# Kernel optimization log

Measured on AMD Instinct MI355X. Metric: run time of the kernel, lower is better.

The kernel has to match this reference:

```python
import jax, jax.numpy as jnp
import numpy as np

E = 512      # embed_size
H = 8        # heads
HD = E // H  # head_dim
TN = 288     # time_num
FE = 4       # forward_expansion
N, T = 64, 512


def layernorm(x, g, b, eps=1e-5):
    mu = jnp.mean(x, axis=-1, keepdims=True)
    var = jnp.mean((x - mu) ** 2, axis=-1, keepdims=True)
    return (x - mu) * jax.lax.rsqrt(var + eps) * g + b


def setup_inputs() -> dict:
    key = jax.random.key(0)
    ks = jax.random.split(key, 12)
    w = lambda k, sh: jax.random.normal(k, sh, dtype=jnp.float32) * 0.02
    return {
        "value": jax.random.normal(ks[0], (N, T, E), dtype=jnp.float32),
        "key_in": jax.random.normal(ks[1], (N, T, E), dtype=jnp.float32),
        "query": jax.random.normal(ks[2], (N, T, E), dtype=jnp.float32),
        "i": 37,
        # One_hot_encoder params: learned identity-init table + linear to embed
        "I_mat": jnp.eye(TN, dtype=jnp.float32),
        "oh_W": w(ks[3], (TN, E)), "oh_b": jnp.zeros((E,), jnp.float32),
        # per-head projections (shared across heads, as in the torch module)
        "Wv": w(ks[4], (HD, HD)), "Wk": w(ks[5], (HD, HD)), "Wq": w(ks[6], (HD, HD)),
        "Wo": w(ks[7], (E, E)), "bo": jnp.zeros((E,), jnp.float32),
        "g1": jnp.ones((E,), jnp.float32), "b1": jnp.zeros((E,), jnp.float32),
        "g2": jnp.ones((E,), jnp.float32), "b2": jnp.zeros((E,), jnp.float32),
        "W1": w(ks[8], (E, FE * E)), "bf1": jnp.zeros((FE * E,), jnp.float32),
        "W2": w(ks[9], (FE * E, E)), "bf2": jnp.zeros((E,), jnp.float32),
    }


def reference(value, key_in, query, i, I_mat, oh_W, oh_b, Wv, Wk, Wq, Wo, bo,
              g1, b1, g2, b2, W1, bf1, W2, bf2):
    n, t, c = query.shape
    # One_hot_encoder: rows i..i+T-1 (mod time_num) of learned table -> linear
    rows = (i + jnp.arange(t)) % TN
    onehot = I_mat[rows] @ oh_W + oh_b            # (T, E), broadcast over N
    q_in = query + onehot[None, :, :]
    # per-head projections
    v = value.reshape(n, t, H, HD) @ Wv           # (N,T,H,HD)
    k = key_in.reshape(n, t, H, HD) @ Wk
    qh = q_in.reshape(n, t, H, HD) @ Wq
    # attention (note: scale uses sqrt(embed_size), per original code)
    energy = jnp.einsum("nqhd,nkhd->nhqk", qh, k) / jnp.sqrt(jnp.float32(E))
    attn = jax.nn.softmax(energy, axis=-1)
    out = jnp.einsum("nhqk,nkhd->nqhd", attn, v).reshape(n, t, E)
    out = out @ Wo + bo
    # residual + LN + FFN + residual + LN (dropout=0 -> identity)
    x = layernorm(out + q_in, g1, b1)
    ff = jax.nn.relu(x @ W1 + bf1) @ W2 + bf2
    return layernorm(ff + x, g2, b2)
```

## Files before the change

kernel.cpp:

```cpp
#include <hip/hip_runtime.h>

typedef __attribute__((ext_vector_type(8))) short s16x8;
typedef __attribute__((ext_vector_type(4))) float f32x4;

#define TN 288

__device__ __forceinline__ unsigned short f2bf(float f) {
  union { float f; unsigned u; } v; v.f = f;
  unsigned r = v.u + 0x7fffu + ((v.u >> 16) & 1u);
  return (unsigned short)(r >> 16);
}
__device__ __forceinline__ float bf2f(unsigned short u) {
  union { float f; unsigned u; } v; v.u = ((unsigned)u) << 16;
  return v.f;
}
__device__ __forceinline__ unsigned lds_addr(const void* p) {
  return (unsigned)(unsigned long long)(const __attribute__((address_space(3))) char*)p;
}
__device__ __forceinline__ void async_copy16(unsigned short* lds, const unsigned short* g) {
  __builtin_amdgcn_global_load_lds(
      (const __attribute__((address_space(1))) unsigned int*)g,
      (__attribute__((address_space(3))) unsigned int*)lds, 16, 0, 0);
}

__device__ __forceinline__ void pack_body(const float* __restrict__ W,
    unsigned short* __restrict__ out, int N, long t) {
  int lr = (int)(t & 15);
  int lg = (int)((t >> 4) & 3);
  long g6 = t >> 6;
  int nt = N >> 4;
  int n16 = (int)(g6 % nt);
  int kb = (int)(g6 / nt) << 5;
  int k = kb + lg * 8;
  int col = n16 * 16 + lr;
  s16x8 v;
#pragma unroll
  for (int j = 0; j < 8; ++j) v[j] = (short)f2bf(W[(size_t)(k + j) * N + col]);
  *(s16x8*)(out + t * 8) = v;
}

__global__ __launch_bounds__(256) void prep_kernel(const int* __restrict__ pi,
    const float* __restrict__ I_mat, const float* __restrict__ ohW,
    const float* __restrict__ ohb, float* __restrict__ onehot,
    const float* __restrict__ Wv, const float* __restrict__ Wk,
    const float* __restrict__ Wq, unsigned short* __restrict__ Wv_b,
    unsigned short* __restrict__ Wk_b, unsigned short* __restrict__ Wq_b,
    const float* __restrict__ Wo, const float* __restrict__ W1,
    const float* __restrict__ W2, unsigned short* __restrict__ Wop,
    unsigned short* __restrict__ W1p, unsigned short* __restrict__ W2p) {
  int b = blockIdx.x, tid = threadIdx.x;
  if (b < 512) {
    int t = b;
    int r = (pi[0] + t) % TN;
    float acc0 = ohb[tid], acc1 = ohb[tid + 256];
    const float* Ir = I_mat + (size_t)r * TN;
    for (int j = 0; j < TN; ++j) {
      float iv = Ir[j];
      acc0 += iv * ohW[(size_t)j * 512 + tid];
      acc1 += iv * ohW[(size_t)j * 512 + tid + 256];
    }
    onehot[(size_t)t * 512 + tid] = acc0;
    onehot[(size_t)t * 512 + tid + 256] = acc1;
  } else if (b < 640) {
    pack_body(Wo, Wop, 512, (long)(b - 512) * 256 + tid);
  } else if (b < 1152) {
    pack_body(W1, W1p, 2048, (long)(b - 640) * 256 + tid);
  } else if (b < 1664) {
    pack_body(W2, W2p, 512, (long)(b - 1152) * 256 + tid);
  } else {
    int which = b - 1664;
    const float* src = which == 0 ? Wv : (which == 1 ? Wk : Wq);
    unsigned short* dst = which == 0 ? Wv_b : (which == 1 ? Wk_b : Wq_b);
    float sc = which == 2 ? 0.06375871424f : 1.f;
#pragma unroll
    for (int j = 0; j < 4; ++j) {
      int i = tid * 16 + j * 4;
      float4 f = *(const float4*)(src + i);
      unsigned lo = (unsigned)f2bf(f.x * sc) | ((unsigned)f2bf(f.y * sc) << 16);
      unsigned hi = (unsigned)f2bf(f.z * sc) | ((unsigned)f2bf(f.w * sc) << 16);
      *(uint2*)(dst + i) = make_uint2(lo, hi);
    }
  }
}

template<bool QIN, int OUTMODE>
__global__ __launch_bounds__(256) void proj_gemm(const float* __restrict__ A,
    const unsigned short* __restrict__ B, const float* __restrict__ onehot,
    unsigned short* __restrict__ C, int M, int N, int K) {
  __shared__ unsigned short As[64][40];
  __shared__ unsigned short Bs[64][40];
  __shared__ unsigned short Cs[64][72];
  const int m0 = blockIdx.x * 64, n0 = blockIdx.y * 64;
  const int tid = threadIdx.x, w = tid >> 6, l = tid & 63, lr = l & 15, lg = l >> 4;
  const int wr = (w >> 1) * 32, wc = (w & 1) * 32;
  const int aRow = (tid * 8) >> 5, aK = (tid * 8) & 31;
  const int bK = (tid * 8) >> 6, bCol = (tid * 8) & 63;
  f32x4 acc[2][2] = {};
  for (int kb = 0; kb < K; kb += 32) {
    size_t fl = (size_t)(m0 + aRow) * K + kb + aK;
    float4 f0 = *(const float4*)(A + fl);
    float4 f1 = *(const float4*)(A + fl + 4);
    if (QIN) {
      const float* oh = onehot + (fl & 262143);
      float4 o0 = *(const float4*)(oh);
      float4 o1 = *(const float4*)(oh + 4);
      f0.x += o0.x; f0.y += o0.y; f0.z += o0.z; f0.w += o0.w;
      f1.x += o1.x; f1.y += o1.y; f1.z += o1.z; f1.w += o1.w;
    }
    s16x8 av;
    av[0] = (short)f2bf(f0.x); av[1] = (short)f2bf(f0.y);
    av[2] = (short)f2bf(f0.z); av[3] = (short)f2bf(f0.w);
    av[4] = (short)f2bf(f1.x); av[5] = (short)f2bf(f1.y);
    av[6] = (short)f2bf(f1.z); av[7] = (short)f2bf(f1.w);
    *(s16x8*)&As[aRow][aK] = av;
    s16x8 bv = *(const s16x8*)(B + (size_t)(kb + bK) * N + n0 + bCol);
#pragma unroll
    for (int j = 0; j < 8; ++j) Bs[bCol + j][bK] = (unsigned short)bv[j];
    __syncthreads();
    s16x8 af0 = *(const s16x8*)&As[wr + lr][lg * 8];
    s16x8 af1 = *(const s16x8*)&As[wr + 16 + lr][lg * 8];
    s16x8 bf0 = *(const s16x8*)&Bs[wc + lr][lg * 8];
    s16x8 bf1 = *(const s16x8*)&Bs[wc + 16 + lr][lg * 8];
    acc[0][0] = __builtin_amdgcn_mfma_f32_16x16x32_bf16(af0, bf0, acc[0][0], 0, 0, 0);
    acc[0][1] = __builtin_amdgcn_mfma_f32_16x16x32_bf16(af0, bf1, acc[0][1], 0, 0, 0);
    acc[1][0] = __builtin_amdgcn_mfma_f32_16x16x32_bf16(af1, bf0, acc[1][0], 0, 0, 0);
    acc[1][1] = __builtin_amdgcn_mfma_f32_16x16x32_bf16(af1, bf1, acc[1][1], 0, 0, 0);
    __syncthreads();
  }
  if (OUTMODE == 0) {
#pragma unroll
    for (int fi = 0; fi < 2; ++fi)
#pragma unroll
      for (int fj = 0; fj < 2; ++fj)
#pragma unroll
        for (int r = 0; r < 4; ++r) {
          int row = m0 + wr + fi * 16 + lg * 4 + r;
          int col = n0 + wc + fj * 16 + lr;
          C[(size_t)row * N + col] = f2bf(acc[fi][fj][r]);
        }
  } else {
#pragma unroll
    for (int fi = 0; fi < 2; ++fi)
#pragma unroll
      for (int fj = 0; fj < 2; ++fj)
#pragma unroll
        for (int r = 0; r < 4; ++r)
          Cs[wr + fi * 16 + lg * 4 + r][wc + fj * 16 + lr] = f2bf(acc[fi][fj][r]);
    __syncthreads();
    int nIdx = m0 >> 12, t0 = (m0 >> 3) & 511;
#pragma unroll
    for (int it = 0; it < 2; ++it) {
      int p = tid + it * 256;
      int hh = p >> 6, d = p & 63;
      s16x8 vv;
#pragma unroll
      for (int j = 0; j < 8; ++j) vv[j] = (short)Cs[j * 8 + hh][d];
      *(s16x8*)(C + (((size_t)(nIdx * 8 + hh) * 64 + d) << 9) + t0) = vv;
    }
  }
}

template<bool RELU, bool OUTBF>
__global__ __launch_bounds__(256) void gemmF(
    const unsigned short* __restrict__ A, int lda,
    const unsigned short* __restrict__ Bp, int ldbp, int nOff,
    const float* __restrict__ bias, void* __restrict__ Cout, int ldc,
    int M, int K, int nby) {
  __shared__ unsigned short As[2][8192];
  const int tid = threadIdx.x, w = tid >> 6, l = tid & 63, lr = l & 15, lg = l >> 4;
  const int nwg = gridDim.x;
  const int bid = (blockIdx.x & 7) * (nwg >> 3) + (blockIdx.x >> 3);
  const int bx = bid / nby, by = bid % nby;
  const int m0 = bx * 128;
  const int wr = (w >> 1) * 64, wc = (w & 1) * 64;
  const int srow = tid >> 3, sc8 = tid & 7;
  const int gcol = (sc8 ^ (srow & 7)) * 8;
  const unsigned short* Ag = A + (size_t)(m0 + srow) * lda + gcol;
  const size_t ldaa = (size_t)32 * lda;
  const unsigned short* Bg = Bp +
      ((size_t)(nOff >> 4) + by * 8 + (wc >> 4)) * 512 + lg * 128 + lr * 8;
  const size_t bks = (size_t)ldbp * 512;

  f32x4 acc[4][4] = {};
  s16x8 b0[4], b1[4];

#pragma unroll
  for (int it = 0; it < 4; ++it)
    async_copy16(&As[0][(it * 256 + tid) * 8], Ag + it * ldaa);
#pragma unroll
  for (int fj = 0; fj < 4; ++fj) {
    b0[fj] = *(const s16x8*)(Bg + fj * 512);
    b1[fj] = *(const s16x8*)(Bg + bks + fj * 512);
  }
  __syncthreads();

  int buf = 0;
  for (int kb = 0; kb < K; kb += 64) {
    int kn = (kb + 64 < K) ? kb + 64 : 0;
#pragma unroll
    for (int it = 0; it < 4; ++it)
      async_copy16(&As[buf ^ 1][(it * 256 + tid) * 8], Ag + kn + it * ldaa);
    s16x8 b0n[4];
    {
      const unsigned short* p = Bg + ((size_t)(kn >> 5)) * bks;
#pragma unroll
      for (int fj = 0; fj < 4; ++fj) b0n[fj] = *(const s16x8*)(p + fj * 512);
    }
    {
      s16x8 af[4];
#pragma unroll
      for (int fi = 0; fi < 4; ++fi) {
        int row = wr + fi * 16 + lr;
        af[fi] = *(const s16x8*)&As[buf][row * 64 + ((lg ^ (row & 7)) * 8)];
      }
#pragma unroll
      for (int fi = 0; fi < 4; ++fi)
#pragma unroll
        for (int fj = 0; fj < 4; ++fj)
          acc[fi][fj] = __builtin_amdgcn_mfma_f32_16x16x32_bf16(af[fi], b0[fj], acc[fi][fj], 0, 0, 0);
    }
    s16x8 b1n[4];
    {
      const unsigned short* p = Bg + ((size_t)((kn + 32) >> 5)) * bks;
#pragma unroll
      for (int fj = 0; fj < 4; ++fj) b1n[fj] = *(const s16x8*)(p + fj * 512);
    }
    {
      s16x8 af[4];
#pragma unroll
      for (int fi = 0; fi < 4; ++fi) {
        int row = wr + fi * 16 + lr;
        af[fi] = *(const s16x8*)&As[buf][row * 64 + (((4 + lg) ^ (row & 7)) * 8)];
      }
#pragma unroll
      for (int fi = 0; fi < 4; ++fi)
#pragma unroll
        for (int fj = 0; fj < 4; ++fj)
          acc[fi][fj] = __builtin_amdgcn_mfma_f32_16x16x32_bf16(af[fi], b1[fj], acc[fi][fj], 0, 0, 0);
    }
    __syncthreads();
#pragma unroll
    for (int fj = 0; fj < 4; ++fj) { b0[fj] = b0n[fj]; b1[fj] = b1n[fj]; }
    buf ^= 1;
  }

#pragma unroll
  for (int fj = 0; fj < 4; ++fj) {
    int colL = by * 128 + wc + fj * 16 + lr;
    float bv = bias[nOff + colL];
#pragma unroll
    for (int fi = 0; fi < 4; ++fi)
#pragma unroll
      for (int r = 0; r < 4; ++r) {
        int row = m0 + wr + fi * 16 + lg * 4 + r;
        size_t ci = (size_t)row * ldc + colL;
        float v = acc[fi][fj][r] + bv;
        if (RELU) v = fmaxf(v, 0.f);
        if (OUTBF) ((unsigned short*)Cout)[ci] = f2bf(v);
        else ((float*)Cout)[ci] = v;
      }
  }
}

__global__ __launch_bounds__(256, 2) void attn_kernel(
    const unsigned short* __restrict__ Qp, const unsigned short* __restrict__ Kp,
    const unsigned short* __restrict__ Vt, unsigned short* __restrict__ Out) {
  __shared__ unsigned short KS[128][72];
  __shared__ unsigned short P[4][16][132];
  const int bid = blockIdx.x;
  const int qh = bid >> 9, g = bid & 511, h = g & 7, n = g >> 3;
  const int tid = threadIdx.x, w = tid >> 6, l = tid & 63, lr = l & 15, lg = l >> 4;
  const int q0 = qh * 256;

  s16x8 qf[4][2];
#pragma unroll
  for (int rt = 0; rt < 4; ++rt) {
    const size_t qb = (((size_t)(n * 512 + q0 + w * 64 + rt * 16 + lr)) * 8 + h) * 64;
    qf[rt][0] = *(const s16x8*)(Qp + qb + lg * 8);
    qf[rt][1] = *(const s16x8*)(Qp + qb + 32 + lg * 8);
  }
  const unsigned short* Vb = Vt + ((size_t)(n * 8 + h)) * 32768 + (size_t)lr * 512 + lg * 8;

  f32x4 oacc[4][4] = {};
  float m[4][4], lsum[4][4];
#pragma unroll
  for (int rt = 0; rt < 4; ++rt)
#pragma unroll
    for (int r = 0; r < 4; ++r) { m[rt][r] = -1e30f; lsum[rt][r] = 0.f; }
  s16x8 vreg[16];

#pragma unroll
  for (int it = 0; it < 4; ++it) {
    int idx = tid + it * 256;
    int rr = idx >> 3, dd = (idx & 7) * 8;
    *(s16x8*)&KS[rr][dd] =
        *(const s16x8*)(Kp + (((size_t)(n * 512 + rr)) * 8 + h) * 64 + dd);
  }
#pragma unroll
  for (int ks = 0; ks < 4; ++ks)
#pragma unroll
    for (int fj = 0; fj < 4; ++fj)
      vreg[ks * 4 + fj] = *(const s16x8*)(Vb + fj * 8192 + ks * 32);
  __syncthreads();

  for (int c = 0; c < 4; ++c) {
    if (c) {
      __syncthreads();
#pragma unroll
      for (int it = 0; it < 4; ++it) {
        int idx = tid + it * 256;
        int rr = idx >> 3, dd = (idx & 7) * 8;
        *(s16x8*)&KS[rr][dd] =
            *(const s16x8*)(Kp + (((size_t)(n * 512 + c * 128 + rr)) * 8 + h) * 64 + dd);
      }
#pragma unroll
      for (int ks = 0; ks < 4; ++ks)
#pragma unroll
        for (int fj = 0; fj < 4; ++fj)
          vreg[ks * 4 + fj] = *(const s16x8*)(Vb + fj * 8192 + c * 128 + ks * 32);
      __syncthreads();
    }
#pragma unroll
    for (int rt = 0; rt < 4; ++rt) {
      f32x4 sacc[8];
      __builtin_amdgcn_s_setprio(1);
#pragma unroll
      for (int f = 0; f < 8; ++f) {
        s16x8 b0 = *(const s16x8*)&KS[f * 16 + lr][lg * 8];
        s16x8 b1 = *(const s16x8*)&KS[f * 16 + lr][32 + lg * 8];
        f32x4 a = {};
        a = __builtin_amdgcn_mfma_f32_16x16x32_bf16(qf[rt][0], b0, a, 0, 0, 0);
        a = __builtin_amdgcn_mfma_f32_16x16x32_bf16(qf[rt][1], b1, a, 0, 0, 0);
        sacc[f] = a;
      }
      __builtin_amdgcn_s_setprio(0);

      float fs[4];
#pragma unroll
      for (int r = 0; r < 4; ++r) {
        float cm = sacc[0][r];
#pragma unroll
        for (int f = 1; f < 8; ++f) cm = fmaxf(cm, sacc[f][r]);
#pragma unroll
        for (int mk = 1; mk < 16; mk <<= 1) cm = fmaxf(cm, __shfl_xor(cm, mk));
        float mn = fmaxf(m[rt][r], cm);
        fs[r] = __builtin_amdgcn_exp2f(m[rt][r] - mn);
        m[rt][r] = mn;
        unsigned pa = lds_addr(&P[w][lg * 4 + r][lr]);
        float cs = 0.f;
#pragma unroll
        for (int f = 0; f < 8; ++f) {
          float p = __builtin_amdgcn_exp2f(sacc[f][r] - mn);
          asm volatile("ds_write_b16_d16_hi %0, %1 offset:%2"
                       :: "v"(pa), "v"(p), "i"(f * 32) : "memory");
          cs += p;
        }
#pragma unroll
        for (int mk = 1; mk < 16; mk <<= 1) cs += __shfl_xor(cs, mk);
        lsum[rt][r] = lsum[rt][r] * fs[r] + cs;
      }
#pragma unroll
      for (int fj = 0; fj < 4; ++fj)
#pragma unroll
        for (int r = 0; r < 4; ++r) oacc[rt][fj][r] *= fs[r];

      asm volatile("s_waitcnt lgkmcnt(0)" ::: "memory");
      __builtin_amdgcn_sched_barrier(0);
      __builtin_amdgcn_s_setprio(1);
#pragma unroll
      for (int ks = 0; ks < 4; ++ks) {
        s16x8 pa = *(const s16x8*)&P[w][lr][ks * 32 + lg * 8];
#pragma unroll
        for (int fj = 0; fj < 4; ++fj)
          oacc[rt][fj] = __builtin_amdgcn_mfma_f32_16x16x32_bf16(pa, vreg[ks * 4 + fj], oacc[rt][fj], 0, 0, 0);
      }
      __builtin_amdgcn_s_setprio(0);
    }
  }

#pragma unroll
  for (int rt = 0; rt < 4; ++rt)
#pragma unroll
    for (int fj = 0; fj < 4; ++fj)
#pragma unroll
      for (int r = 0; r < 4; ++r) {
        int qrow = q0 + w * 64 + rt * 16 + lg * 4 + r;
        Out[((size_t)(n * 512 + qrow)) * 512 + h * 64 + fj * 16 + lr] =
            f2bf(oacc[rt][fj][r] / lsum[rt][r]);
      }
}

template<bool XBF, bool RBF, bool QIN, bool OUTBF>
__global__ __launch_bounds__(256) void ln_kernel(const void* __restrict__ Xv,
    const void* __restrict__ Rv, const float* __restrict__ onehot,
    const float* __restrict__ g, const float* __restrict__ bb,
    void* __restrict__ outv) {
  int row = blockIdx.x * 4 + (threadIdx.x >> 6);
  int l = threadIdx.x & 63;
  size_t base = (size_t)row * 512 + l * 8;
  float v[8];
  if (XBF) {
    s16x8 xv = *(const s16x8*)((const unsigned short*)Xv + base);
#pragma unroll
    for (int j = 0; j < 8; ++j) v[j] = bf2f((unsigned short)xv[j]);
  } else {
    const float* X = (const float*)Xv;
    float4 x0 = *(const float4*)(X + base);
    float4 x1 = *(const float4*)(X + base + 4);
    v[0] = x0.x; v[1] = x0.y; v[2] = x0.z; v[3] = x0.w;
    v[4] = x1.x; v[5] = x1.y; v[6] = x1.z; v[7] = x1.w;
  }
  if (RBF) {
    s16x8 rv = *(const s16x8*)((const unsigned short*)Rv + base);
#pragma unroll
    for (int j = 0; j < 8; ++j) v[j] += bf2f((unsigned short)rv[j]);
  } else {
    const float* R = (const float*)Rv;
    float4 r0 = *(const float4*)(R + base);
    float4 r1 = *(const float4*)(R + base + 4);
    v[0] += r0.x; v[1] += r0.y; v[2] += r0.z; v[3] += r0.w;
    v[4] += r1.x; v[5] += r1.y; v[6] += r1.z; v[7] += r1.w;
  }
  if (QIN) {
    size_t ob = (size_t)(row & 511) * 512 + l * 8;
    float4 o0 = *(const float4*)(onehot + ob);
    float4 o1 = *(const float4*)(onehot + ob + 4);
    v[0] += o0.x; v[1] += o0.y; v[2] += o0.z; v[3] += o0.w;
    v[4] += o1.x; v[5] += o1.y; v[6] += o1.z; v[7] += o1.w;
  }
  float s = 0.f, ss = 0.f;
#pragma unroll
  for (int j = 0; j < 8; ++j) { s += v[j]; ss += v[j] * v[j]; }
#pragma unroll
  for (int mk = 1; mk < 64; mk <<= 1) { s += __shfl_xor(s, mk); ss += __shfl_xor(ss, mk); }
  float mu = s * (1.f / 512.f);
  float inv = rsqrtf(ss * (1.f / 512.f) - mu * mu + 1e-5f);
#pragma unroll
  for (int j = 0; j < 8; ++j) {
    int e = l * 8 + j;
    float y = (v[j] - mu) * inv * g[e] + bb[e];
    if (OUTBF) ((unsigned short*)outv)[base + j] = f2bf(y);
    else ((float*)outv)[base + j] = y;
  }
}

extern "C" void kernel_launch(void* const* d_in, const int* in_sizes, int n_in,
                              void* d_out, int out_size, void* d_ws, size_t ws_size,
                              hipStream_t stream) {
  const float* value  = (const float*)d_in[0];
  const float* key_in = (const float*)d_in[1];
  const float* query  = (const float*)d_in[2];
  const int*   pi     = (const int*)d_in[3];
  const float* I_mat  = (const float*)d_in[4];
  const float* ohW    = (const float*)d_in[5];
  const float* ohb    = (const float*)d_in[6];
  const float* Wv     = (const float*)d_in[7];
  const float* Wk     = (const float*)d_in[8];
  const float* Wq     = (const float*)d_in[9];
  const float* Wo     = (const float*)d_in[10];
  const float* bo     = (const float*)d_in[11];
  const float* g1     = (const float*)d_in[12];
  const float* b1     = (const float*)d_in[13];
  const float* g2     = (const float*)d_in[14];
  const float* b2     = (const float*)d_in[15];
  const float* W1     = (const float*)d_in[16];
  const float* bf1    = (const float*)d_in[17];
  const float* W2     = (const float*)d_in[18];
  const float* bf2    = (const float*)d_in[19];

  char* ws = (char*)d_ws;
  const size_t MB = 1024 * 1024;
  unsigned short* q_p  = (unsigned short*)d_out;
  unsigned short* k_p  = q_p + 16777216;
  unsigned short* vT     = (unsigned short*)(ws + 0);
  unsigned short* attn_o = (unsigned short*)(ws + 32 * MB);
  unsigned short* x_b    = (unsigned short*)(ws + 64 * MB);
  unsigned short* ff1h   = (unsigned short*)(ws + 0);
  float*          onehot = (float*)(ws + 96 * MB);
  unsigned short* Wv_b   = (unsigned short*)(ws + 97 * MB);
  unsigned short* Wk_b   = Wv_b + 4096;
  unsigned short* Wq_b   = Wk_b + 4096;
  unsigned short* Wop    = Wq_b + 4096;
  unsigned short* W1p    = Wop + 262144;
  unsigned short* W2p    = W1p + 1048576;

  prep_kernel<<<1667, 256, 0, stream>>>(pi, I_mat, ohW, ohb, onehot,
      Wv, Wk, Wq, Wv_b, Wk_b, Wq_b, Wo, W1, W2, Wop, W1p, W2p);

  dim3 gp(4096, 1);
  proj_gemm<false, 1><<<gp, 256, 0, stream>>>(value,  Wv_b, nullptr, vT,  262144, 64, 64);
  proj_gemm<false, 0><<<gp, 256, 0, stream>>>(key_in, Wk_b, nullptr, k_p, 262144, 64, 64);
  proj_gemm<true,  0><<<gp, 256, 0, stream>>>(query,  Wq_b, onehot,  q_p, 262144, 64, 64);

  attn_kernel<<<1024, 256, 0, stream>>>(q_p, k_p, vT, attn_o);

  gemmF<false, true><<<1024, 256, 0, stream>>>(
      attn_o, 512, Wop, 32, 0, bo, x_b, 512, 32768, 512, 4);
  ln_kernel<true, false, true, true><<<8192, 256, 0, stream>>>(x_b, query, onehot, g1, b1, x_b);

  for (int hf = 0; hf < 2; ++hf) {
    const unsigned short* xh = x_b + (size_t)hf * 16384 * 512;
    gemmF<true, true><<<2048, 256, 0, stream>>>(
        xh, 512, W1p, 128, 0, bf1, ff1h, 2048, 16384, 512, 16);
    gemmF<false, false><<<512, 256, 0, stream>>>(
        ff1h, 2048, W2p, 32, 0, bf2, (float*)d_out + (size_t)hf * 16384 * 512, 512, 16384, 2048, 4);
  }
  ln_kernel<false, true, false, false><<<8192, 256, 0, stream>>>(d_out, x_b, nullptr, g2, b2, d_out);
}
```

Baseline: 468.3 us.

## Merge projection launches, fuse FFN residual into GEMM epilogue, skip unit rescale

Replaces the three projection GEMM launches with one kernel that picks value, key or query from the block index. The second FFN GEMM now adds the bf16 residual in its epilogue, so the final layernorm no longer reads the residual tensor. The attention kernel skips rescaling the output accumulators when every correction factor in the wavefront is exactly one. The aim is fewer launches, less residual traffic and fewer multiplies, at the cost of runtime branching in the projection kernel and a wave-vote check in the softmax loop.

```diff
diff --git a/kernel.cpp b/kernel.cpp
--- a/kernel.cpp
+++ b/kernel.cpp
@@ -83,24 +83,32 @@
   }
 }
 
-template<bool QIN, int OUTMODE>
-__global__ __launch_bounds__(256) void proj_gemm(const float* __restrict__ A,
-    const unsigned short* __restrict__ B, const float* __restrict__ onehot,
-    unsigned short* __restrict__ C, int M, int N, int K) {
+__global__ __launch_bounds__(256) void proj_all(
+    const float* __restrict__ value, const float* __restrict__ key_in,
+    const float* __restrict__ query, const unsigned short* __restrict__ Wv_b,
+    const unsigned short* __restrict__ Wk_b, const unsigned short* __restrict__ Wq_b,
+    const float* __restrict__ onehot, unsigned short* __restrict__ vT,
+    unsigned short* __restrict__ k_p, unsigned short* __restrict__ q_p) {
   __shared__ unsigned short As[64][40];
   __shared__ unsigned short Bs[64][40];
   __shared__ unsigned short Cs[64][72];
-  const int m0 = blockIdx.x * 64, n0 = blockIdx.y * 64;
+  const int which = blockIdx.x >> 12;
+  const int mb = blockIdx.x & 4095;
+  const float* A = which == 0 ? value : (which == 1 ? key_in : query);
+  const unsigned short* B = which == 0 ? Wv_b : (which == 1 ? Wk_b : Wq_b);
+  unsigned short* C = which == 0 ? vT : (which == 1 ? k_p : q_p);
+  const bool qin = (which == 2);
+  const int m0 = mb * 64;
   const int tid = threadIdx.x, w = tid >> 6, l = tid & 63, lr = l & 15, lg = l >> 4;
   const int wr = (w >> 1) * 32, wc = (w & 1) * 32;
   const int aRow = (tid * 8) >> 5, aK = (tid * 8) & 31;
   const int bK = (tid * 8) >> 6, bCol = (tid * 8) & 63;
   f32x4 acc[2][2] = {};
-  for (int kb = 0; kb < K; kb += 32) {
-    size_t fl = (size_t)(m0 + aRow) * K + kb + aK;
+  for (int kb = 0; kb < 64; kb += 32) {
+    size_t fl = (size_t)(m0 + aRow) * 64 + kb + aK;
     float4 f0 = *(const float4*)(A + fl);
     float4 f1 = *(const float4*)(A + fl + 4);
-    if (QIN) {
+    if (qin) {
       const float* oh = onehot + (fl & 262143);
       float4 o0 = *(const float4*)(oh);
       float4 o1 = *(const float4*)(oh + 4);
@@ -113,7 +121,7 @@
     av[4] = (short)f2bf(f1.x); av[5] = (short)f2bf(f1.y);
     av[6] = (short)f2bf(f1.z); av[7] = (short)f2bf(f1.w);
     *(s16x8*)&As[aRow][aK] = av;
-    s16x8 bv = *(const s16x8*)(B + (size_t)(kb + bK) * N + n0 + bCol);
+    s16x8 bv = *(const s16x8*)(B + (size_t)(kb + bK) * 64 + bCol);
 #pragma unroll
     for (int j = 0; j < 8; ++j) Bs[bCol + j][bK] = (unsigned short)bv[j];
     __syncthreads();
@@ -127,7 +135,7 @@
     acc[1][1] = __builtin_amdgcn_mfma_f32_16x16x32_bf16(af1, bf1, acc[1][1], 0, 0, 0);
     __syncthreads();
   }
-  if (OUTMODE == 0) {
+  if (which != 0) {
 #pragma unroll
     for (int fi = 0; fi < 2; ++fi)
 #pragma unroll
@@ -135,8 +143,8 @@
 #pragma unroll
         for (int r = 0; r < 4; ++r) {
           int row = m0 + wr + fi * 16 + lg * 4 + r;
-          int col = n0 + wc + fj * 16 + lr;
-          C[(size_t)row * N + col] = f2bf(acc[fi][fj][r]);
+          int col = wc + fj * 16 + lr;
+          C[(size_t)row * 64 + col] = f2bf(acc[fi][fj][r]);
         }
   } else {
 #pragma unroll
@@ -160,11 +168,12 @@
   }
 }
 
-template<bool RELU, bool OUTBF>
+template<bool RELU, bool OUTBF, bool RES>
 __global__ __launch_bounds__(256) void gemmF(
     const unsigned short* __restrict__ A, int lda,
     const unsigned short* __restrict__ Bp, int ldbp, int nOff,
-    const float* __restrict__ bias, void* __restrict__ Cout, int ldc,
+    const float* __restrict__ bias, void* __restrict__ Cout,
+    const unsigned short* __restrict__ resid, int ldc,
     int M, int K, int nby) {
   __shared__ unsigned short As[2][8192];
   const int tid = threadIdx.x, w = tid >> 6, l = tid & 63, lr = l & 15, lg = l >> 4;
@@ -255,6 +264,7 @@
         int row = m0 + wr + fi * 16 + lg * 4 + r;
         size_t ci = (size_t)row * ldc + colL;
         float v = acc[fi][fj][r] + bv;
+        if (RES) v += bf2f(resid[ci]);
         if (RELU) v = fmaxf(v, 0.f);
         if (OUTBF) ((unsigned short*)Cout)[ci] = f2bf(v);
         else ((float*)Cout)[ci] = v;
@@ -359,10 +369,12 @@
         for (int mk = 1; mk < 16; mk <<= 1) cs += __shfl_xor(cs, mk);
         lsum[rt][r] = lsum[rt][r] * fs[r] + cs;
       }
-#pragma unroll
-      for (int fj = 0; fj < 4; ++fj)
-#pragma unroll
-        for (int r = 0; r < 4; ++r) oacc[rt][fj][r] *= fs[r];
+      if (!__all(fs[0] == 1.f && fs[1] == 1.f && fs[2] == 1.f && fs[3] == 1.f)) {
+#pragma unroll
+        for (int fj = 0; fj < 4; ++fj)
+#pragma unroll
+          for (int r = 0; r < 4; ++r) oacc[rt][fj][r] *= fs[r];
+      }
 
       asm volatile("s_waitcnt lgkmcnt(0)" ::: "memory");
       __builtin_amdgcn_sched_barrier(0);
@@ -390,7 +402,7 @@
       }
 }
 
-template<bool XBF, bool RBF, bool QIN, bool OUTBF>
+template<bool XBF, bool RES, bool RBF, bool QIN, bool OUTBF>
 __global__ __launch_bounds__(256) void ln_kernel(const void* __restrict__ Xv,
     const void* __restrict__ Rv, const float* __restrict__ onehot,
     const float* __restrict__ g, const float* __restrict__ bb,
@@ -410,16 +422,18 @@
     v[0] = x0.x; v[1] = x0.y; v[2] = x0.z; v[3] = x0.w;
     v[4] = x1.x; v[5] = x1.y; v[6] = x1.z; v[7] = x1.w;
   }
-  if (RBF) {
-    s16x8 rv = *(const s16x8*)((const unsigned short*)Rv + base);
-#pragma unroll
-    for (int j = 0; j < 8; ++j) v[j] += bf2f((unsigned short)rv[j]);
-  } else {
-    const float* R = (const float*)Rv;
-    float4 r0 = *(const float4*)(R + base);
-    float4 r1 = *(const float4*)(R + base + 4);
-    v[0] += r0.x; v[1] += r0.y; v[2] += r0.z; v[3] += r0.w;
-    v[4] += r1.x; v[5] += r1.y; v[6] += r1.z; v[7] += r1.w;
+  if (RES) {
+    if (RBF) {
+      s16x8 rv = *(const s16x8*)((const unsigned short*)Rv + base);
+#pragma unroll
+      for (int j = 0; j < 8; ++j) v[j] += bf2f((unsigned short)rv[j]);
+    } else {
+      const float* R = (const float*)Rv;
+      float4 r0 = *(const float4*)(R + base);
+      float4 r1 = *(const float4*)(R + base + 4);
+      v[0] += r0.x; v[1] += r0.y; v[2] += r0.z; v[3] += r0.w;
+      v[4] += r1.x; v[5] += r1.y; v[6] += r1.z; v[7] += r1.w;
+    }
   }
   if (QIN) {
     size_t ob = (size_t)(row & 511) * 512 + l * 8;
@@ -487,23 +501,24 @@
   prep_kernel<<<1667, 256, 0, stream>>>(pi, I_mat, ohW, ohb, onehot,
       Wv, Wk, Wq, Wv_b, Wk_b, Wq_b, Wo, W1, W2, Wop, W1p, W2p);
 
-  dim3 gp(4096, 1);
-  proj_gemm<false, 1><<<gp, 256, 0, stream>>>(value,  Wv_b, nullptr, vT,  262144, 64, 64);
-  proj_gemm<false, 0><<<gp, 256, 0, stream>>>(key_in, Wk_b, nullptr, k_p, 262144, 64, 64);
-  proj_gemm<true,  0><<<gp, 256, 0, stream>>>(query,  Wq_b, onehot,  q_p, 262144, 64, 64);
+  proj_all<<<12288, 256, 0, stream>>>(value, key_in, query,
+      Wv_b, Wk_b, Wq_b, onehot, vT, k_p, q_p);
 
   attn_kernel<<<1024, 256, 0, stream>>>(q_p, k_p, vT, attn_o);
 
-  gemmF<false, true><<<1024, 256, 0, stream>>>(
-      attn_o, 512, Wop, 32, 0, bo, x_b, 512, 32768, 512, 4);
-  ln_kernel<true, false, true, true><<<8192, 256, 0, stream>>>(x_b, query, onehot, g1, b1, x_b);
+  gemmF<false, true, false><<<1024, 256, 0, stream>>>(
+      attn_o, 512, Wop, 32, 0, bo, x_b, nullptr, 512, 32768, 512, 4);
+  ln_kernel<true, true, false, true, true><<<8192, 256, 0, stream>>>(
+      x_b, query, onehot, g1, b1, x_b);
 
   for (int hf = 0; hf < 2; ++hf) {
     const unsigned short* xh = x_b + (size_t)hf * 16384 * 512;
-    gemmF<true, true><<<2048, 256, 0, stream>>>(
-        xh, 512, W1p, 128, 0, bf1, ff1h, 2048, 16384, 512, 16);
-    gemmF<false, false><<<512, 256, 0, stream>>>(
-        ff1h, 2048, W2p, 32, 0, bf2, (float*)d_out + (size_t)hf * 16384 * 512, 512, 16384, 2048, 4);
-  }
-  ln_kernel<false, true, false, false><<<8192, 256, 0, stream>>>(d_out, x_b, nullptr, g2, b2, d_out);
-}
+    gemmF<true, true, false><<<2048, 256, 0, stream>>>(
+        xh, 512, W1p, 128, 0, bf1, ff1h, nullptr, 2048, 16384, 512, 16);
+    gemmF<false, false, true><<<512, 256, 0, stream>>>(
+        ff1h, 2048, W2p, 32, 0, bf2, (float*)d_out + (size_t)hf * 16384 * 512,
+        xh, 512, 16384, 2048, 4);
+  }
+  ln_kernel<false, false, false, false, false><<<8192, 256, 0, stream>>>(
+      d_out, nullptr, nullptr, g2, b2, d_out);
+}
```

After: 500.8 us. 1.07x slower.
